# Performance work log

Measured on AMD Instinct MI355X. Metric: run time of the kernel, lower is better.

The kernel has to match this reference:

```python
import jax, jax.numpy as jnp
import numpy as np

T, B, A, OBS = 128, 16, 32, 256
K, NACT, HID = 3, 9, 32


def setup_inputs() -> dict:
    key = jax.random.key(0)
    ks = jax.random.split(key, 12)
    sc = 0.1  # small init scale for stability
    d = {}
    d["x"] = jax.random.normal(ks[0], (T, B, A, OBS), jnp.float32)
    d["done"] = jax.random.randint(ks[1], (T, B), 0, 2, jnp.int32)
    d["actions"] = jax.random.randint(ks[2], (T, B, A, K), 0, NACT, jnp.int32)
    d["W1"] = sc * jax.random.normal(ks[3], (128, OBS), jnp.float32)
    d["b1"] = jnp.zeros((128,), jnp.float32)
    d["W2"] = sc * jax.random.normal(ks[4], (128, 128), jnp.float32)
    d["b2"] = jnp.zeros((128,), jnp.float32)
    d["W3"] = sc * jax.random.normal(ks[5], (64, 128), jnp.float32)
    d["b3"] = jnp.zeros((64,), jnp.float32)
    d["Wih"] = sc * jax.random.normal(ks[6], (4 * HID, 64), jnp.float32)
    d["Whh"] = sc * jax.random.normal(ks[7], (4 * HID, HID), jnp.float32)
    d["bih"] = jnp.zeros((4 * HID,), jnp.float32)
    d["bhh"] = jnp.zeros((4 * HID,), jnp.float32)
    d["Wh"] = sc * jax.random.normal(ks[8], (K, NACT, HID), jnp.float32)
    d["bh"] = jnp.zeros((K, NACT), jnp.float32)
    d["h0"] = jnp.zeros((B * A, HID), jnp.float32)
    d["c0"] = jnp.zeros((B * A, HID), jnp.float32)
    return d


def _forward(x, done, actions, W1, b1, W2, b2, W3, b3,
             Wih, Whh, bih, bhh, Wh, bh, h0, c0):
    # MLP trunk: n_obs -> 128 -> 128 -> 64 (tanh, tanh, linear)
    z = jnp.tanh(x @ W1.T + b1)
    z = jnp.tanh(z @ W2.T + b2)
    z = z @ W3.T + b3                       # [T, B, A, 64]
    zf = z.reshape(T, B * A, 64)
    # done[t] repeated per agent (repeat_interleave along batch*agent axis)
    done_f = jnp.repeat(done.astype(x.dtype), A, axis=1)  # [T, B*A]

    def step(carry, inp):
        h, c = carry
        zt, dt = inp                        # [B*A,64], [B*A]
        mask = (1.0 - dt)[:, None]
        h = h * mask
        c = c * mask
        gates = zt @ Wih.T + bih + h @ Whh.T + bhh  # [B*A, 4H]
        i, f, g, o = jnp.split(gates, 4, axis=-1)   # PyTorch gate order i,f,g,o
        i, f, o = jax.nn.sigmoid(i), jax.nn.sigmoid(f), jax.nn.sigmoid(o)
        g = jnp.tanh(g)
        c = f * c + i * g
        h = o * jnp.tanh(c)
        return (h, c), h

    (_, _), ys = jax.lax.scan(step, (h0, c0), (zf, done_f))
    y = ys.reshape(T, B, A, HID)
    # multi-head categorical logits: stacked heads [K, NACT, HID]
    logits = jnp.einsum('tbah,knh->tbakn', y, Wh) + bh  # [T,B,A,K,NACT]
    lp = jax.nn.log_softmax(logits, axis=-1)
    entropies = -jnp.sum(jnp.exp(lp) * lp, axis=-1)     # [T,B,A,K]
    alp = jnp.take_along_axis(lp, actions[..., None], axis=-1)[..., 0]  # [T,B,A,K]
    logprobs = jnp.prod(alp, axis=-1)  # faithful: product of per-head log-probs
    return logprobs, entropies


def reference(x, done, actions, W1, b1, W2, b2, W3, b3,
              Wih, Whh, bih, bhh, Wh, bh, h0, c0):
    logprobs, entropies = _forward(x, done, actions, W1, b1, W2, b2, W3, b3,
                                   Wih, Whh, bih, bhh, Wh, bh, h0, c0)
    return actions, logprobs, entropies
```

## Files before the change

### kernel.cpp

```cpp
#include <hip/hip_runtime.h>
#include <math.h>

namespace {
constexpr int Tn = 128, Bn = 16, An = 32, OBS = 256, Kh = 3, NACT = 9, HID = 32;
constexpr int TBA = Tn * Bn * An;
constexpr int BA  = Bn * An;
constexpr int OUT_LP  = TBA * Kh;
constexpr int OUT_ENT = TBA * Kh + TBA;

constexpr int W1_OFF  = 0;
constexpr int W2_OFF  = 32768;
constexpr int W3_OFF  = 49152;
constexpr int WIH_OFF = 57344;
constexpr int W16_TOT = 65536;

typedef __fp16   pk16x2 __attribute__((ext_vector_type(2)));
typedef _Float16 half8v __attribute__((ext_vector_type(8)));
typedef float    f32x4  __attribute__((ext_vector_type(4)));
}

__device__ __forceinline__ float fast_sig(float x) {
  return __builtin_amdgcn_rcpf(1.f + __expf(-x));
}
__device__ __forceinline__ float fast_tanh(float x) {
  return fmaf(2.f, fast_sig(2.f * x), -1.f);
}
__device__ __forceinline__ unsigned h2bits(pk16x2 h) {
  return __builtin_bit_cast(unsigned, h);
}
__device__ __forceinline__ pk16x2 bits2h(unsigned u) {
  return __builtin_bit_cast(pk16x2, u);
}
__device__ __forceinline__ float dot2(pk16x2 a, pk16x2 b, float c) {
#if __has_builtin(__builtin_amdgcn_fdot2)
  return __builtin_amdgcn_fdot2(a, b, c, false);
#else
  c = fmaf((float)a.x, (float)b.x, c);
  return fmaf((float)a.y, (float)b.y, c);
#endif
}
__device__ __forceinline__ float dpp_swap1(float x) {
  return __uint_as_float((unsigned)__builtin_amdgcn_mov_dpp(
      (int)__float_as_uint(x), 0xB1, 0xF, 0xF, true));
}

__global__ __launch_bounds__(256) void cvtw_act_kernel(
    const float* __restrict__ W1, const float* __restrict__ W2,
    const float* __restrict__ W3, const float* __restrict__ Wih,
    _Float16* __restrict__ w16, const int* __restrict__ actions,
    float* __restrict__ out)
{
  const int bid = blockIdx.x;
  if (bid < W16_TOT/256) {
    int i = bid * 256 + threadIdx.x;
    float v;
    if (i < W2_OFF)       v = W1[i];
    else if (i < W3_OFF)  v = W2[i - W2_OFF];
    else if (i < WIH_OFF) v = W3[i - W3_OFF];
    else                  v = Wih[i - WIH_OFF];
    w16[i] = (_Float16)v;
  } else {
    int i = (bid - W16_TOT/256) * 256 + threadIdx.x;
    out[i] = (float)actions[i];
  }
}

template<int ROWS, int WSTR>
__device__ __forceinline__ void stage_wh(const _Float16* __restrict__ Wg, int kofs,
                                         _Float16* __restrict__ wt, int tid)
{
#pragma unroll
  for (int it = 0; it < ROWS/64; ++it) {
    int idx = tid + it*512;
    int o = idx >> 3, g8 = idx & 7;
    *(half8v*)&wt[o*72 + g8*8] =
        *(const half8v*)&Wg[(size_t)o*WSTR + kofs + g8*8];
  }
}

template<int NOC, int XSTR>
__device__ __forceinline__ void mfma_slab(const _Float16* __restrict__ xsrc,
                                          const _Float16* __restrict__ wt,
                                          int rA, int ln, int quad, f32x4 acc[8])
{
#pragma unroll
  for (int kc = 0; kc < 2; ++kc) {
    half8v a = *(const half8v*)&xsrc[rA*XSTR + kc*32 + quad*8];
#pragma unroll
    for (int oc = 0; oc < NOC; ++oc) {
      half8v b = *(const half8v*)&wt[(oc*16 + ln)*72 + kc*32 + quad*8];
      acc[oc] = __builtin_amdgcn_mfma_f32_16x16x32_f16(a, b, acc[oc], 0, 0, 0);
    }
  }
}

__global__ __launch_bounds__(512) void mlp_kernel(
    const float* __restrict__ x, const _Float16* __restrict__ w16,
    const float* __restrict__ b1, const float* __restrict__ b2,
    const float* __restrict__ b3, const float* __restrict__ bih,
    const float* __restrict__ bhh, uint2* __restrict__ G1q)
{
  __shared__ __align__(16) _Float16 xs[128*72];
  __shared__ __align__(16) _Float16 wt[128*72];
  __shared__ __align__(16) _Float16 act[128*136];
  const _Float16* W1h  = w16 + W1_OFF;
  const _Float16* W2h  = w16 + W2_OFF;
  const _Float16* W3h  = w16 + W3_OFF;
  const _Float16* Wihh = w16 + WIH_OFF;
  const int tid  = threadIdx.x;
  const int w    = tid >> 6;
  const int lane = tid & 63;
  const int ln   = lane & 15;
  const int quad = lane >> 4;
  const int rA   = 16*w + ln;
  const int r0   = 16*w + quad*4;
  const int R0   = blockIdx.x * 128;
  f32x4 acc[8];

#pragma unroll
  for (int oc = 0; oc < 8; ++oc) acc[oc] = (f32x4)0.f;
  for (int kt = 0; kt < 4; ++kt) {
#pragma unroll
    for (int it = 0; it < 2; ++it) {
      int idx = tid + it*512;
      int r = idx >> 3, g8 = idx & 7;
      const float* xp = &x[(size_t)(R0 + r)*OBS + kt*64 + g8*8];
      float4 v0 = *(const float4*)xp;
      float4 v1 = *(const float4*)(xp + 4);
      half8v hv = { (_Float16)v0.x, (_Float16)v0.y, (_Float16)v0.z, (_Float16)v0.w,
                    (_Float16)v1.x, (_Float16)v1.y, (_Float16)v1.z, (_Float16)v1.w };
      *(half8v*)&xs[r*72 + g8*8] = hv;
    }
    stage_wh<128, 256>(W1h, kt*64, wt, tid);
    __syncthreads();
    mfma_slab<8, 72>(xs, wt, rA, ln, quad, acc);
    __syncthreads();
  }
#pragma unroll
  for (int oc = 0; oc < 8; ++oc) {
    int o = oc*16 + ln;
    float bv = b1[o];
#pragma unroll
    for (int r = 0; r < 4; ++r)
      act[(r0 + r)*136 + o] = (_Float16)fast_tanh(acc[oc][r] + bv);
  }

#pragma unroll
  for (int oc = 0; oc < 8; ++oc) acc[oc] = (f32x4)0.f;
  for (int kt = 0; kt < 2; ++kt) {
    stage_wh<128, 128>(W2h, kt*64, wt, tid);
    __syncthreads();
    mfma_slab<8, 136>(act + kt*64, wt, rA, ln, quad, acc);
    __syncthreads();
  }
#pragma unroll
  for (int oc = 0; oc < 8; ++oc) {
    int o = oc*16 + ln;
    float bv = b2[o];
#pragma unroll
    for (int r = 0; r < 4; ++r)
      act[(r0 + r)*136 + o] = (_Float16)fast_tanh(acc[oc][r] + bv);
  }

#pragma unroll
  for (int oc = 0; oc < 4; ++oc) acc[oc] = (f32x4)0.f;
  for (int kt = 0; kt < 2; ++kt) {
    stage_wh<64, 128>(W3h, kt*64, wt, tid);
    __syncthreads();
    mfma_slab<4, 136>(act + kt*64, wt, rA, ln, quad, acc);
    __syncthreads();
  }
#pragma unroll
  for (int oc = 0; oc < 4; ++oc) {
    int o = oc*16 + ln;
    float bv = b3[o];
#pragma unroll
    for (int r = 0; r < 4; ++r)
      xs[(r0 + r)*72 + o] = (_Float16)(acc[oc][r] + bv);
  }

#pragma unroll
  for (int oc = 0; oc < 8; ++oc) acc[oc] = (f32x4)0.f;
  stage_wh<128, 64>(Wihh, 0, wt, tid);
  __syncthreads();
  mfma_slab<8, 72>(xs, wt, rA, ln, quad, acc);
#pragma unroll
  for (int p = 0; p < 2; ++p) {
    int ui = p*16 + ln;
    float bi = bih[ui]      + bhh[ui];
    float bf = bih[ui + 32] + bhh[ui + 32];
    float bg = bih[ui + 64] + bhh[ui + 64];
    float bo = bih[ui + 96] + bhh[ui + 96];
#pragma unroll
    for (int r = 0; r < 4; ++r) {
      int n = R0 + r0 + r;
      uint2 q;
      q.x = h2bits(__builtin_amdgcn_cvt_pkrtz(acc[p  ][r] + bi, acc[p+4][r] + bg));
      q.y = h2bits(__builtin_amdgcn_cvt_pkrtz(acc[p+2][r] + bf, acc[p+6][r] + bo));
      G1q[(size_t)n*32 + ui] = q;
    }
  }
}

__global__ __launch_bounds__(64) void lstm_kernel(
    const uint2* __restrict__ G1q, const float* __restrict__ Whh,
    const int* __restrict__ done, const float* __restrict__ h0,
    const float* __restrict__ c0, unsigned* __restrict__ Y16)
{
  const int lane = threadIdx.x;
  const int u = lane & 31;
  const int row = blockIdx.x;
  const int b = row >> 5;

  pk16x2 wi[16], wf[16], wg[16], wo[16];
#pragma unroll
  for (int k4 = 0; k4 < 8; ++k4) {
    float4 a  = *(const float4*)&Whh[(u      )*HID + k4*4];
    float4 bq = *(const float4*)&Whh[(u + 32 )*HID + k4*4];
    float4 cq = *(const float4*)&Whh[(u + 64 )*HID + k4*4];
    float4 dq = *(const float4*)&Whh[(u + 96 )*HID + k4*4];
    wi[2*k4+0] = __builtin_amdgcn_cvt_pkrtz(a.x,  a.y);
    wi[2*k4+1] = __builtin_amdgcn_cvt_pkrtz(a.z,  a.w);
    wf[2*k4+0] = __builtin_amdgcn_cvt_pkrtz(bq.x, bq.y);
    wf[2*k4+1] = __builtin_amdgcn_cvt_pkrtz(bq.z, bq.w);
    wg[2*k4+0] = __builtin_amdgcn_cvt_pkrtz(cq.x, cq.y);
    wg[2*k4+1] = __builtin_amdgcn_cvt_pkrtz(cq.z, cq.w);
    wo[2*k4+0] = __builtin_amdgcn_cvt_pkrtz(dq.x, dq.y);
    wo[2*k4+1] = __builtin_amdgcn_cvt_pkrtz(dq.z, dq.w);
  }

  unsigned long long dm0 = __ballot(done[lane*Bn + b] != 0);
  unsigned long long dm1 = __ballot(done[(lane + 64)*Bn + b] != 0);

  float c = c0[row*HID + u];
  float h = h0[row*HID + u];
  unsigned pk = h2bits(__builtin_amdgcn_cvt_pkrtz(h, dpp_swap1(h)));

  const uint2* gbase = G1q + (size_t)row*32 + u;
  const size_t gstride = (size_t)BA*32;
  uint2 q0 = gbase[0*gstride];
  uint2 q1 = gbase[1*gstride];
  uint2 q2 = gbase[2*gstride];
  uint2 q3 = gbase[3*gstride];
  uint2 q4 = gbase[4*gstride];
  uint2 q5 = gbase[5*gstride];
  uint2 q6 = gbase[6*gstride];
  uint2 q7 = gbase[7*gstride];

#define LSTM_PHASE(TT, Q)                                                \
  {                                                                      \
    uint2 cur = Q;                                                       \
    int tnx = (TT) + 8; tnx = (tnx < Tn) ? tnx : (Tn - 1);               \
    Q = gbase[(size_t)tnx * gstride];                                    \
    unsigned long long dbit = ((TT) < 64) ? (dm0 >> (TT))                \
                                          : (dm1 >> ((TT) - 64));        \
    float m = (dbit & 1ull) ? 0.f : 1.f;         \
    unsigned hp[16];                                                     \
    _Pragma("unroll") for (int k = 0; k < 16; ++k)                       \
      hp[k] = __builtin_amdgcn_readlane(pk, 2*k);                        \
    float ai0=0.f, ai1=0.f, af0=0.f, af1=0.f;                            \
    float ag0=0.f, ag1=0.f, ao0=0.f, ao1=0.f;                            \
    _Pragma("unroll") for (int k = 0; k < 16; k += 2) {                  \
      pk16x2 ha = bits2h(hp[k]), hb = bits2h(hp[k+1]);                   \
      ai0 = dot2(wi[k], ha, ai0); ai1 = dot2(wi[k+1], hb, ai1);          \
      af0 = dot2(wf[k], ha, af0); af1 = dot2(wf[k+1], hb, af1);          \
      ag0 = dot2(wg[k], ha, ag0); ag1 = dot2(wg[k+1], hb, ag1);          \
      ao0 = dot2(wo[k], ha, ao0); ao1 = dot2(wo[k+1], hb, ao1);          \
    }                                                                    \
    pk16x2 ig = bits2h(cur.x), fo = bits2h(cur.y);                       \
    float gi = fmaf(m, ai0 + ai1, (float)ig.x);                          \
    float gf = fmaf(m, af0 + af1, (float)fo.x);                          \
    float gg = fmaf(m, ag0 + ag1, (float)ig.y);                          \
    float go = fmaf(m, ao0 + ao1, (float)fo.y);                          \
    float iv = fast_sig(gi), fv = fast_sig(gf);                          \
    float gv = fast_tanh(gg), ov = fast_sig(go);                         \
    c = fmaf(fv, m * c, iv * gv);                                        \
    h = ov * fast_tanh(c);                                               \
    pk = h2bits(__builtin_amdgcn_cvt_pkrtz(h, dpp_swap1(h)));            \
    if ((lane & 33) == 0)                                                \
      Y16[((size_t)(TT)*BA + row)*16 + (u >> 1)] = pk;                   \
  }

  for (int t = 0; t < Tn; t += 8) {
    LSTM_PHASE(t + 0, q0)
    LSTM_PHASE(t + 1, q1)
    LSTM_PHASE(t + 2, q2)
    LSTM_PHASE(t + 3, q3)
    LSTM_PHASE(t + 4, q4)
    LSTM_PHASE(t + 5, q5)
    LSTM_PHASE(t + 6, q6)
    LSTM_PHASE(t + 7, q7)
  }
#undef LSTM_PHASE
}

__global__ __launch_bounds__(256) void head_kernel(
    const unsigned* __restrict__ Y16, const float* __restrict__ Wh,
    const float* __restrict__ bh, const int* __restrict__ actions,
    float* __restrict__ out)
{
  __shared__ __align__(16) float whs[27*32];
  __shared__ float bhs[32];
  const int tid = threadIdx.x;
  const int R0 = blockIdx.x * 256;
  for (int i = tid; i < 27*32; i += 256) whs[i] = Wh[i];
  if (tid < 27) bhs[tid] = bh[tid];
  const int row = R0 + tid;
  float yv[32];
#pragma unroll
  for (int i4 = 0; i4 < 4; ++i4) {
    uint4 yw = *(const uint4*)&Y16[(size_t)row*16 + i4*4];
    pk16x2 p0 = bits2h(yw.x), p1 = bits2h(yw.y), p2 = bits2h(yw.z), p3 = bits2h(yw.w);
    yv[i4*8+0] = (float)p0.x; yv[i4*8+1] = (float)p0.y;
    yv[i4*8+2] = (float)p1.x; yv[i4*8+3] = (float)p1.y;
    yv[i4*8+4] = (float)p2.x; yv[i4*8+5] = (float)p2.y;
    yv[i4*8+6] = (float)p3.x; yv[i4*8+7] = (float)p3.y;
  }
  __syncthreads();
  float l[27];
#pragma unroll
  for (int m = 0; m < 27; ++m) {
    float a = bhs[m];
#pragma unroll
    for (int k4 = 0; k4 < 8; ++k4) {
      float4 w4 = *(const float4*)&whs[m*32 + k4*4];
      a = fmaf(yv[k4*4+0], w4.x, a);
      a = fmaf(yv[k4*4+1], w4.y, a);
      a = fmaf(yv[k4*4+2], w4.z, a);
      a = fmaf(yv[k4*4+3], w4.w, a);
    }
    l[m] = a;
  }
  float logprob = 1.0f;
#pragma unroll
  for (int kk = 0; kk < 3; ++kk) {
    float mx = l[kk*9];
#pragma unroll
    for (int n = 1; n < 9; ++n) mx = fmaxf(mx, l[kk*9+n]);
    float s = 0.f;
#pragma unroll
    for (int n = 0; n < 9; ++n) s += __expf(l[kk*9+n] - mx);
    float lse = mx + __logf(s);
    float ent = 0.f;
#pragma unroll
    for (int n = 0; n < 9; ++n) {
      float lp = l[kk*9+n] - lse;
      ent -= __expf(lp) * lp;
    }
    int a = actions[row*3 + kk];
    float alp = 0.f;
#pragma unroll
    for (int n = 0; n < 9; ++n) alp = (a == n) ? (l[kk*9+n] - lse) : alp;
    logprob *= alp;
    out[OUT_ENT + row*3 + kk] = ent;
  }
  out[OUT_LP + row] = logprob;
}

extern "C" void kernel_launch(void* const* d_in, const int* in_sizes, int n_in,
                              void* d_out, int out_size, void* d_ws, size_t ws_size,
                              hipStream_t stream)
{
  const float* x       = (const float*)d_in[0];
  const int*   done    = (const int*)  d_in[1];
  const int*   actions = (const int*)  d_in[2];
  const float* W1  = (const float*)d_in[3];
  const float* b1  = (const float*)d_in[4];
  const float* W2  = (const float*)d_in[5];
  const float* b2  = (const float*)d_in[6];
  const float* W3  = (const float*)d_in[7];
  const float* b3  = (const float*)d_in[8];
  const float* Wih = (const float*)d_in[9];
  const float* Whh = (const float*)d_in[10];
  const float* bih = (const float*)d_in[11];
  const float* bhh = (const float*)d_in[12];
  const float* Wh  = (const float*)d_in[13];
  const float* bh  = (const float*)d_in[14];
  const float* h0  = (const float*)d_in[15];
  const float* c0  = (const float*)d_in[16];
  float* out = (float*)d_out;

  uint2* G1q = (uint2*)d_ws;
  unsigned* Y16 = (unsigned*)(G1q + (size_t)TBA*32);
  _Float16* W16 = (_Float16*)(Y16 + (size_t)TBA*16);

  cvtw_act_kernel<<<W16_TOT/256 + (TBA*Kh)/256, 256, 0, stream>>>(
      W1, W2, W3, Wih, W16, actions, out);
  mlp_kernel<<<TBA/128, 512, 0, stream>>>(x, W16, b1, b2, b3, bih, bhh, G1q);
  lstm_kernel<<<BA, 64, 0, stream>>>(G1q, Whh, done, h0, c0, Y16);
  head_kernel<<<TBA/256, 256, 0, stream>>>(Y16, Wh, bh, actions, out);
}
```

Before: 194.3 us.

## Split LSTM gate work across both wave halves and deepen gate prefetch

The 64-lane LSTM wave previously computed all four gates redundantly in both 32-lane halves. Now each half owns two gate rows: i/g for the low half and f/o for the high half. Tanh is computed as a scaled sigmoid, and the gate values are exchanged with a cross-half shuffle. The per-step dot-product work and weight registers are halved, at the cost of a shuffle on the serial critical path. The input-gate prefetch depth also doubles from 8 to 16 steps.

```diff
diff --git a/kernel.cpp b/kernel.cpp
--- a/kernel.cpp
+++ b/kernel.cpp
@@ -208,25 +208,21 @@
     const float* __restrict__ c0, unsigned* __restrict__ Y16)
 {
   const int lane = threadIdx.x;
-  const int u = lane & 31;
-  const int row = blockIdx.x;
-  const int b = row >> 5;
-
-  pk16x2 wi[16], wf[16], wg[16], wo[16];
+  const int u    = lane & 31;
+  const int half = lane >> 5;
+  const int row  = blockIdx.x;
+  const int b    = row >> 5;
+
+  pk16x2 wA[16], wB[16];
+  const int rwA = u + half*32;
 #pragma unroll
   for (int k4 = 0; k4 < 8; ++k4) {
-    float4 a  = *(const float4*)&Whh[(u      )*HID + k4*4];
-    float4 bq = *(const float4*)&Whh[(u + 32 )*HID + k4*4];
-    float4 cq = *(const float4*)&Whh[(u + 64 )*HID + k4*4];
-    float4 dq = *(const float4*)&Whh[(u + 96 )*HID + k4*4];
-    wi[2*k4+0] = __builtin_amdgcn_cvt_pkrtz(a.x,  a.y);
-    wi[2*k4+1] = __builtin_amdgcn_cvt_pkrtz(a.z,  a.w);
-    wf[2*k4+0] = __builtin_amdgcn_cvt_pkrtz(bq.x, bq.y);
-    wf[2*k4+1] = __builtin_amdgcn_cvt_pkrtz(bq.z, bq.w);
-    wg[2*k4+0] = __builtin_amdgcn_cvt_pkrtz(cq.x, cq.y);
-    wg[2*k4+1] = __builtin_amdgcn_cvt_pkrtz(cq.z, cq.w);
-    wo[2*k4+0] = __builtin_amdgcn_cvt_pkrtz(dq.x, dq.y);
-    wo[2*k4+1] = __builtin_amdgcn_cvt_pkrtz(dq.z, dq.w);
+    float4 a  = *(const float4*)&Whh[(rwA     )*HID + k4*4];
+    float4 bq = *(const float4*)&Whh[(rwA + 64)*HID + k4*4];
+    wA[2*k4+0] = __builtin_amdgcn_cvt_pkrtz(a.x,  a.y);
+    wA[2*k4+1] = __builtin_amdgcn_cvt_pkrtz(a.z,  a.w);
+    wB[2*k4+0] = __builtin_amdgcn_cvt_pkrtz(bq.x, bq.y);
+    wB[2*k4+1] = __builtin_amdgcn_cvt_pkrtz(bq.z, bq.w);
   }
 
   unsigned long long dm0 = __ballot(done[lane*Bn + b] != 0);
@@ -236,44 +232,57 @@
   float h = h0[row*HID + u];
   unsigned pk = h2bits(__builtin_amdgcn_cvt_pkrtz(h, dpp_swap1(h)));
 
-  const uint2* gbase = G1q + (size_t)row*32 + u;
-  const size_t gstride = (size_t)BA*32;
-  uint2 q0 = gbase[0*gstride];
-  uint2 q1 = gbase[1*gstride];
-  uint2 q2 = gbase[2*gstride];
-  uint2 q3 = gbase[3*gstride];
-  uint2 q4 = gbase[4*gstride];
-  uint2 q5 = gbase[5*gstride];
-  uint2 q6 = gbase[6*gstride];
-  uint2 q7 = gbase[7*gstride];
+  const float sSc = half ? 1.f : 2.f;
+  const float m1c = half ? 1.f : 2.f;
+  const float m0c = half ? 0.f : -1.f;
+
+  const unsigned* gb = (const unsigned*)G1q + ((size_t)row*32 + u)*2 + half;
+  const size_t gstride = (size_t)BA * 64;
+  unsigned q0  = gb[ 0*gstride];
+  unsigned q1  = gb[ 1*gstride];
+  unsigned q2  = gb[ 2*gstride];
+  unsigned q3  = gb[ 3*gstride];
+  unsigned q4  = gb[ 4*gstride];
+  unsigned q5  = gb[ 5*gstride];
+  unsigned q6  = gb[ 6*gstride];
+  unsigned q7  = gb[ 7*gstride];
+  unsigned q8  = gb[ 8*gstride];
+  unsigned q9  = gb[ 9*gstride];
+  unsigned q10 = gb[10*gstride];
+  unsigned q11 = gb[11*gstride];
+  unsigned q12 = gb[12*gstride];
+  unsigned q13 = gb[13*gstride];
+  unsigned q14 = gb[14*gstride];
+  unsigned q15 = gb[15*gstride];
 
 #define LSTM_PHASE(TT, Q)                                                \
   {                                                                      \
-    uint2 cur = Q;                                                       \
-    int tnx = (TT) + 8; tnx = (tnx < Tn) ? tnx : (Tn - 1);               \
-    Q = gbase[(size_t)tnx * gstride];                                    \
+    unsigned cur = Q;                                                    \
+    int tnx = (TT) + 16; tnx = (tnx < Tn) ? tnx : (Tn - 1);              \
+    Q = gb[(size_t)tnx * gstride];                                       \
     unsigned long long dbit = ((TT) < 64) ? (dm0 >> (TT))                \
                                           : (dm1 >> ((TT) - 64));        \
     float m = (dbit & 1ull) ? 0.f : 1.f;         \
     unsigned hp[16];                                                     \
     _Pragma("unroll") for (int k = 0; k < 16; ++k)                       \
       hp[k] = __builtin_amdgcn_readlane(pk, 2*k);                        \
-    float ai0=0.f, ai1=0.f, af0=0.f, af1=0.f;                            \
-    float ag0=0.f, ag1=0.f, ao0=0.f, ao1=0.f;                            \
+    float aA0=0.f, aA1=0.f, aB0=0.f, aB1=0.f;                            \
     _Pragma("unroll") for (int k = 0; k < 16; k += 2) {                  \
       pk16x2 ha = bits2h(hp[k]), hb = bits2h(hp[k+1]);                   \
-      ai0 = dot2(wi[k], ha, ai0); ai1 = dot2(wi[k+1], hb, ai1);          \
-      af0 = dot2(wf[k], ha, af0); af1 = dot2(wf[k+1], hb, af1);          \
-      ag0 = dot2(wg[k], ha, ag0); ag1 = dot2(wg[k+1], hb, ag1);          \
-      ao0 = dot2(wo[k], ha, ao0); ao1 = dot2(wo[k+1], hb, ao1);          \
+      aA0 = dot2(wA[k], ha, aA0); aA1 = dot2(wA[k+1], hb, aA1);          \
+      aB0 = dot2(wB[k], ha, aB0); aB1 = dot2(wB[k+1], hb, aB1);          \
     }                                                                    \
-    pk16x2 ig = bits2h(cur.x), fo = bits2h(cur.y);                       \
-    float gi = fmaf(m, ai0 + ai1, (float)ig.x);                          \
-    float gf = fmaf(m, af0 + af1, (float)fo.x);                          \
-    float gg = fmaf(m, ag0 + ag1, (float)ig.y);                          \
-    float go = fmaf(m, ao0 + ao1, (float)fo.y);                          \
-    float iv = fast_sig(gi), fv = fast_sig(gf);                          \
-    float gv = fast_tanh(gg), ov = fast_sig(go);                         \
+    pk16x2 g2 = bits2h(cur);                                             \
+    float x0 = fmaf(m, aA0 + aA1, (float)g2.x);               \
+    float x1 = fmaf(m, aB0 + aB1, (float)g2.y);               \
+    float v0 = fast_sig(x0);                                             \
+    float v1 = fmaf(m1c, fast_sig(sSc * x1), m0c);                       \
+    float o0 = __shfl_xor(v0, 32, 64);                                   \
+    float o1 = __shfl_xor(v1, 32, 64);                                   \
+    float iv = half ? o0 : v0;                                           \
+    float fv = half ? v0 : o0;                                           \
+    float gv = half ? o1 : v1;                                           \
+    float ov = half ? v1 : o1;                                           \
     c = fmaf(fv, m * c, iv * gv);                                        \
     h = ov * fast_tanh(c);                                               \
     pk = h2bits(__builtin_amdgcn_cvt_pkrtz(h, dpp_swap1(h)));            \
@@ -281,15 +290,23 @@
       Y16[((size_t)(TT)*BA + row)*16 + (u >> 1)] = pk;                   \
   }
 
-  for (int t = 0; t < Tn; t += 8) {
-    LSTM_PHASE(t + 0, q0)
-    LSTM_PHASE(t + 1, q1)
-    LSTM_PHASE(t + 2, q2)
-    LSTM_PHASE(t + 3, q3)
-    LSTM_PHASE(t + 4, q4)
-    LSTM_PHASE(t + 5, q5)
-    LSTM_PHASE(t + 6, q6)
-    LSTM_PHASE(t + 7, q7)
+  for (int t = 0; t < Tn; t += 16) {
+    LSTM_PHASE(t +  0, q0)
+    LSTM_PHASE(t +  1, q1)
+    LSTM_PHASE(t +  2, q2)
+    LSTM_PHASE(t +  3, q3)
+    LSTM_PHASE(t +  4, q4)
+    LSTM_PHASE(t +  5, q5)
+    LSTM_PHASE(t +  6, q6)
+    LSTM_PHASE(t +  7, q7)
+    LSTM_PHASE(t +  8, q8)
+    LSTM_PHASE(t +  9, q9)
+    LSTM_PHASE(t + 10, q10)
+    LSTM_PHASE(t + 11, q11)
+    LSTM_PHASE(t + 12, q12)
+    LSTM_PHASE(t + 13, q13)
+    LSTM_PHASE(t + 14, q14)
+    LSTM_PHASE(t + 15, q15)
   }
 #undef LSTM_PHASE
 }
```

Result: faster. 187.1 us (-3.7%).
